# Kernel tuning notes

Measured on AMD Instinct MI355X. Metric: run time of the kernel, lower is better.

Reference implementation:

```python
import jax, jax.numpy as jnp
import numpy as np

NEG_SLOPE = 0.01  # torch F.leaky_relu default

def _lrelu(x):
    return jax.nn.leaky_relu(x, NEG_SLOPE)

def setup_inputs() -> dict:
    key = jax.random.key(0)
    ks = jax.random.split(key, 24)
    B, N, E = 512, 20000, 640000
    n_enc_1, n_enc_2, n_z = 512, 256, 64
    n_dec_2, n_dec_1, hidden = 256, 512, 256
    p = lambda k, shp, fan: jax.random.normal(k, shp, jnp.float32) * (1.0 / np.sqrt(fan))
    return {
        "data": jax.random.normal(ks[0], (B, N), jnp.float32),
        "noise": jax.random.normal(ks[1], (B, N), jnp.float32),
        "edge_index": jax.random.randint(ks[2], (2, E), 0, N, jnp.int32),
        "w_gcn": jax.random.normal(ks[3], (), jnp.float32),
        "b_gcn": jax.random.normal(ks[4], (), jnp.float32) * 0.1,
        "enc1_w": p(ks[5], (N, n_enc_1), N), "enc1_b": p(ks[6], (n_enc_1,), N),
        "enc2_w": p(ks[7], (n_enc_1, n_enc_2), n_enc_1), "enc2_b": p(ks[8], (n_enc_2,), n_enc_1),
        "enc3_w": p(ks[9], (n_enc_2, n_z), n_enc_2), "enc3_b": p(ks[10], (n_z,), n_enc_2),
        "dec1_w": p(ks[11], (n_z, n_dec_2), n_z), "dec1_b": p(ks[12], (n_dec_2,), n_z),
        "dec2_w": p(ks[13], (n_dec_2, n_dec_1), n_dec_2), "dec2_b": p(ks[14], (n_dec_1,), n_dec_2),
        "dec3_w": p(ks[15], (n_dec_1, N), n_dec_1), "dec3_b": p(ks[16], (N,), n_dec_1),
        "disc1_w": p(ks[17], (n_z, hidden), n_z), "disc1_b": p(ks[18], (hidden,), n_z),
        "disc2_w": p(ks[19], (hidden, hidden), hidden), "disc2_b": p(ks[20], (hidden,), hidden),
        "disc3_w": p(ks[21], (hidden, 1), hidden), "disc3_b": p(ks[22], (1,), hidden),
    }

def _gcn_batched(x, edge_index, w_gcn, b_gcn):
    # x: [B, N] -> GCNConv(1,1, improved=True) applied per row, vectorized.
    B, N = x.shape
    src, dst = edge_index[0], edge_index[1]
    loop = jnp.arange(N, dtype=src.dtype)
    src_a = jnp.concatenate([src, loop])
    dst_a = jnp.concatenate([dst, loop])
    # improved=True: self-loop edge weight 2.0
    ew = jnp.concatenate([jnp.ones(src.shape[0], x.dtype), jnp.full((N,), 2.0, x.dtype)])
    deg = jax.ops.segment_sum(ew, dst_a, num_segments=N)
    dinv = jnp.where(deg > 0, jax.lax.rsqrt(deg), 0.0)
    norm = dinv[src_a] * ew * dinv[dst_a]  # [E+N]
    xl = x * w_gcn                         # lin (1x1 weight, no bias)
    msgs = xl[:, src_a] * norm[None, :]    # [B, E+N]
    agg = jnp.zeros_like(x).at[:, dst_a].add(msgs)
    return agg + b_gcn

def reference(data, noise, edge_index, w_gcn, b_gcn,
              enc1_w, enc1_b, enc2_w, enc2_b, enc3_w, enc3_b,
              dec1_w, dec1_b, dec2_w, dec2_b, dec3_w, dec3_b,
              disc1_w, disc1_b, disc2_w, disc2_b, disc3_w, disc3_b):
    x = data + noise * 0.1
    gcn_out = _lrelu(_gcn_batched(x, edge_index, w_gcn, b_gcn))  # [B, N]
    h1 = _lrelu(gcn_out @ enc1_w + enc1_b)
    h2 = _lrelu(h1 @ enc2_w + enc2_b)
    z = _lrelu(h2 @ enc3_w + enc3_b)
    d1 = _lrelu(z @ dec1_w + dec1_b)
    d2 = _lrelu(d1 @ dec2_w + dec2_b)
    dec_h3 = _lrelu(d2 @ dec3_w + dec3_b)
    g1 = _lrelu(z @ disc1_w + disc1_b)
    g2 = _lrelu(g1 @ disc2_w + disc2_b)
    d = jax.nn.sigmoid(g2 @ disc3_w + disc3_b)
    return (dec_h3, z, d)
```

## Files before the change

### kernel.cpp

```cpp
#include <hip/hip_runtime.h>
#include <hip/hip_bf16.h>


#define LRELU(v) ((v) > 0.f ? (v) : 0.01f * (v))

static constexpr int Bb = 512;
static constexpr int Nn = 20000;
static constexpr int Ee = 640000;
static constexpr int KPAD = 20480;
static constexpr int NPD = 20096;
static constexpr int RSU = 36;
static constexpr int RSW = 18;

typedef __attribute__((ext_vector_type(8))) short short8;
typedef __attribute__((ext_vector_type(4))) short short4v;
typedef __attribute__((ext_vector_type(4))) float f32x4;

__device__ __forceinline__ ushort f2bf(float f) {
  uint u = __builtin_bit_cast(uint, f);
  u = u + 0x7FFFu + ((u >> 16) & 1u);
  return (ushort)(u >> 16);
}
__device__ __forceinline__ float bfLo(uint u) {
  return __builtin_bit_cast(float, u << 16);
}
__device__ __forceinline__ float bfHi(uint u) {
  return __builtin_bit_cast(float, u & 0xffff0000u);
}

__global__ void transpose_xs_k(const float* __restrict__ a, const float* __restrict__ nz,
                               const float* __restrict__ dinv, ushort* __restrict__ xs) {
  __shared__ ushort tile[64][65];
  int c0 = blockIdx.x * 64;
  int p = blockIdx.y;
  int rbase = p * 64;
  for (int i = threadIdx.x; i < 64 * 64; i += 256) {
    int rr = i >> 6, cc = i & 63;
    int r = rbase + rr, c = c0 + cc;
    ushort v = 0;
    if (c < Nn) {
      size_t idx = (size_t)r * Nn + c;
      v = f2bf(dinv[c] * (a[idx] + 0.1f * nz[idx]));
    }
    tile[rr][cc] = v;
  }
  __syncthreads();
  for (int i = threadIdx.x; i < 64 * 64; i += 256) {
    int cc = i >> 6, rr = i & 63;
    int c = c0 + cc;
    if (c < Nn) xs[((size_t)p * Nn + c) * 64 + rr] = tile[rr][cc];
  }
}

__global__ void hist_check_k(const int* __restrict__ src, const int* __restrict__ dst, int E,
                             int* __restrict__ cnt, int* __restrict__ flag) {
  int i = blockIdx.x * 256 + threadIdx.x;
  if (i < E) {
    int s = src[i], d = dst[i];
    if ((unsigned)s >= (unsigned)Nn || (unsigned)d >= (unsigned)Nn) {
      atomicExch(flag, 1);
    } else {
      atomicAdd(&cnt[d], 1);
    }
  }
}

__global__ void offs_k(const int* __restrict__ cnt, int* __restrict__ offs,
                       int* __restrict__ cursor, float* __restrict__ dinv,
                       int* __restrict__ bump) {
  int i = blockIdx.x * 256 + threadIdx.x;
  int l = threadIdx.x & 63;
  int v = (i < Nn) ? cnt[i] : 0;
  int x = v;
#pragma unroll
  for (int d = 1; d < 64; d <<= 1) {
    int t = __shfl_up(x, d);
    if (l >= d) x += t;
  }
  int total = __shfl(x, 63);
  int base = 0;
  if (l == 0) base = atomicAdd(bump, total);
  base = __shfl(base, 0);
  int excl = base + x - v;
  if (i < Nn) {
    offs[i] = excl;
    cursor[i] = excl;
    dinv[i] = rsqrtf(2.0f + (float)v);
  }
}

__global__ void scatter_k(const int* __restrict__ src, const int* __restrict__ dst, int E,
                          int* __restrict__ cursor, uint* __restrict__ eOff) {
  int i = blockIdx.x * 256 + threadIdx.x;
  if (i < E) {
    int s = src[i], d = dst[i];
    if ((unsigned)s >= (unsigned)Nn || (unsigned)d >= (unsigned)Nn) return;
    int p = atomicAdd(&cursor[d], 1);
    eOff[p] = (uint)s * 128u;
  }
}

__global__ __launch_bounds__(256) void spmm_p8_k(
    const ushort* __restrict__ xs, const uint* __restrict__ eOff, const int* __restrict__ offs,
    const int* __restrict__ cnt, const float* __restrict__ dinv, const float* __restrict__ wg,
    const float* __restrict__ bg, ushort* __restrict__ gcnT) {
  __shared__ uint sIdx[4][2][32];
  int bid = blockIdx.x;
  int panel = bid & 7;
  int wv = threadIdx.x >> 6, l = threadIdx.x & 63;
  int h = l >> 5, q = l & 31;
  int n = (bid >> 3) * 8 + wv * 2 + h;
  int o = offs[n], c = cnt[n];
  const char* base = (const char*)(xs + (size_t)panel * Nn * 64) + q * 4;
  const uint* ep = eOff + o;
  uint su = *(const uint*)(base + (size_t)n * 128);
  float a0 = 2.0f * bfLo(su), a1 = 2.0f * bfHi(su);
  float b0 = 0.f, b1 = 0.f;

  for (int bi = 0; bi < c; bi += 32) {
    int rem = c - bi;
    if (rem > 32) rem = 32;
    sIdx[wv][h][q] = (q < rem) ? ep[bi + q] : 0u;
    int i = 0;
    for (; i + 8 <= rem; i += 8) {
      uint u[8];
#pragma unroll
      for (int j = 0; j < 8; ++j) u[j] = *(const uint*)(base + sIdx[wv][h][i + j]);
#pragma unroll
      for (int j = 0; j < 8; j += 2) {
        a0 += bfLo(u[j]);
        a1 += bfHi(u[j]);
        b0 += bfLo(u[j + 1]);
        b1 += bfHi(u[j + 1]);
      }
    }
    for (; i < rem; ++i) {
      uint u = *(const uint*)(base + sIdx[wv][h][i]);
      a0 += bfLo(u);
      a1 += bfHi(u);
    }
  }

  float wdn = wg[0] * dinv[n], bb = bg[0];
  float v0 = wdn * (a0 + b0) + bb;
  float v1 = wdn * (a1 + b1) + bb;
  v0 = LRELU(v0);
  v1 = LRELU(v1);
  uint pk = (uint)f2bf(v0) | ((uint)f2bf(v1) << 16);
  *(uint*)&gcnT[((size_t)panel * KPAD + n) * 64 + 2 * q] = pk;
}

__global__ __launch_bounds__(256) void mfma_gemm3(const ushort* __restrict__ AT,
                                                  const float* __restrict__ B, int ldb, int KB,
                                                  int iters, float* __restrict__ C, int ldc) {
  __shared__ ushort As[128 * RSU];
  __shared__ ushort Bs[128 * RSU];
  int n0 = blockIdx.x * 128, m0 = blockIdx.y * 128;
  int k0 = blockIdx.z * iters * 32;
  int tid = threadIdx.x;
  int kp = tid >> 4;
  int c8 = (tid & 15) * 8;
  int l = tid & 63, w = tid >> 6;
  int wr = w >> 1, wc = w & 1;
  int lrow = l & 15, lkg = l >> 4;
  int gm = m0 + c8;
  const ushort* Ap = AT + (size_t)(gm >> 6) * ((size_t)KPAD * 64) + (gm & 63);
  int bcol = n0 + c8;
  f32x4 acc[4][4] = {};

  uint4 pa0, pa1;
  float4 pb00, pb01, pb10, pb11;

#define GLOAD(KG)                                                              \
  {                                                                            \
    int kq = (KG) + 2 * kp;                                                    \
    pa0 = *(const uint4*)&Ap[(size_t)kq * 64];                                 \
    pa1 = *(const uint4*)&Ap[(size_t)(kq + 1) * 64];                           \
    pb00 = pb01 = pb10 = pb11 = float4{0.f, 0.f, 0.f, 0.f};                    \
    if (kq < KB) {                                                             \
      const float4* bp = (const float4*)(B + (size_t)kq * ldb + bcol);         \
      pb00 = bp[0];                                                            \
      pb01 = bp[1];                                                            \
    }                                                                          \
    if (kq + 1 < KB) {                                                         \
      const float4* bp = (const float4*)(B + (size_t)(kq + 1) * ldb + bcol);   \
      pb10 = bp[0];                                                            \
      pb11 = bp[1];                                                            \
    }                                                                          \
  }

  GLOAD(k0);

  for (int kt = 0; kt < iters; ++kt) {
    uint wa[8], wb[8];
    wa[0] = (pa0.x & 0xffffu) | (pa1.x << 16);
    wa[1] = (pa0.x >> 16) | (pa1.x & 0xffff0000u);
    wa[2] = (pa0.y & 0xffffu) | (pa1.y << 16);
    wa[3] = (pa0.y >> 16) | (pa1.y & 0xffff0000u);
    wa[4] = (pa0.z & 0xffffu) | (pa1.z << 16);
    wa[5] = (pa0.z >> 16) | (pa1.z & 0xffff0000u);
    wa[6] = (pa0.w & 0xffffu) | (pa1.w << 16);
    wa[7] = (pa0.w >> 16) | (pa1.w & 0xffff0000u);
    wb[0] = (uint)f2bf(pb00.x) | ((uint)f2bf(pb10.x) << 16);
    wb[1] = (uint)f2bf(pb00.y) | ((uint)f2bf(pb10.y) << 16);
    wb[2] = (uint)f2bf(pb00.z) | ((uint)f2bf(pb10.z) << 16);
    wb[3] = (uint)f2bf(pb00.w) | ((uint)f2bf(pb10.w) << 16);
    wb[4] = (uint)f2bf(pb01.x) | ((uint)f2bf(pb11.x) << 16);
    wb[5] = (uint)f2bf(pb01.y) | ((uint)f2bf(pb11.y) << 16);
    wb[6] = (uint)f2bf(pb01.z) | ((uint)f2bf(pb11.z) << 16);
    wb[7] = (uint)f2bf(pb01.w) | ((uint)f2bf(pb11.w) << 16);
    __syncthreads();
    {
      uint* aw = (uint*)As;
      uint* bw = (uint*)Bs;
#pragma unroll
      for (int j = 0; j < 8; ++j) {
        aw[(c8 + j) * RSW + kp] = wa[j];
        bw[(c8 + j) * RSW + kp] = wb[j];
      }
    }
    __syncthreads();
    if (kt + 1 < iters) GLOAD(k0 + (kt + 1) * 32);
    short8 a[4], b[4];
#pragma unroll
    for (int mi = 0; mi < 4; ++mi) {
      int m = wr * 64 + mi * 16 + lrow;
      const short4v* p = (const short4v*)&As[m * RSU + lkg * 8];
      a[mi] = __builtin_shufflevector(p[0], p[1], 0, 1, 2, 3, 4, 5, 6, 7);
    }
#pragma unroll
    for (int nj = 0; nj < 4; ++nj) {
      int n = wc * 64 + nj * 16 + lrow;
      const short4v* p = (const short4v*)&Bs[n * RSU + lkg * 8];
      b[nj] = __builtin_shufflevector(p[0], p[1], 0, 1, 2, 3, 4, 5, 6, 7);
    }
#pragma unroll
    for (int mi = 0; mi < 4; ++mi)
#pragma unroll
      for (int nj = 0; nj < 4; ++nj)
        acc[mi][nj] = __builtin_amdgcn_mfma_f32_16x16x32_bf16(a[mi], b[nj], acc[mi][nj], 0, 0, 0);
  }
#undef GLOAD

#pragma unroll
  for (int mi = 0; mi < 4; ++mi)
#pragma unroll
    for (int nj = 0; nj < 4; ++nj)
#pragma unroll
      for (int r = 0; r < 4; ++r) {
        int row = m0 + wr * 64 + mi * 16 + lkg * 4 + r;
        int col = n0 + wc * 64 + nj * 16 + lrow;
        atomicAdd(&C[(size_t)row * ldc + col], acc[mi][nj][r]);
      }
}

__global__ void conv_wf_k(const float* __restrict__ W, ushort* __restrict__ wf) {
  int n = blockIdx.x * 256 + threadIdx.x;
  int kb = blockIdx.y;
  if (n >= NPD) return;
  ushort v[8];
#pragma unroll
  for (int j = 0; j < 8; ++j)
    v[j] = (n < Nn) ? f2bf(W[(size_t)(8 * kb + j) * Nn + n]) : (ushort)0;
  uint4 pk;
  pk.x = (uint)v[0] | ((uint)v[1] << 16);
  pk.y = (uint)v[2] | ((uint)v[3] << 16);
  pk.z = (uint)v[4] | ((uint)v[5] << 16);
  pk.w = (uint)v[6] | ((uint)v[7] << 16);
  *(uint4*)&wf[((size_t)kb * NPD + n) * 8] = pk;
}

__global__ __launch_bounds__(256) void fmg_dec3_k(const ushort* __restrict__ d2f,
                                                  const ushort* __restrict__ wf,
                                                  const float* __restrict__ bias,
                                                  float* __restrict__ C) {
  int n0 = blockIdx.x * 128, m0 = blockIdx.y * 128;
  int l = threadIdx.x & 63, w = threadIdx.x >> 6;
  int wr = w >> 1, wc = w & 1;
  int lrow = l & 15, lkg = l >> 4;
  f32x4 acc[4][4] = {};

#pragma unroll 4
  for (int ks = 0; ks < 16; ++ks) {
    int kb = ks * 4 + lkg;
    short8 a[4], b[4];
#pragma unroll
    for (int mi = 0; mi < 4; ++mi) {
      int m = m0 + wr * 64 + mi * 16 + lrow;
      a[mi] = *(const short8*)&d2f[((size_t)kb * 512 + m) * 8];
    }
#pragma unroll
    for (int nj = 0; nj < 4; ++nj) {
      int n = n0 + wc * 64 + nj * 16 + lrow;
      b[nj] = *(const short8*)&wf[((size_t)kb * NPD + n) * 8];
    }
#pragma unroll
    for (int mi = 0; mi < 4; ++mi)
#pragma unroll
      for (int nj = 0; nj < 4; ++nj)
        acc[mi][nj] = __builtin_amdgcn_mfma_f32_16x16x32_bf16(a[mi], b[nj], acc[mi][nj], 0, 0, 0);
  }

#pragma unroll
  for (int mi = 0; mi < 4; ++mi)
#pragma unroll
    for (int nj = 0; nj < 4; ++nj)
#pragma unroll
      for (int r = 0; r < 4; ++r) {
        int row = m0 + wr * 64 + mi * 16 + lkg * 4 + r;
        int col = n0 + wc * 64 + nj * 16 + lrow;
        if (col < Nn) {
          float v = acc[mi][nj][r] + bias[col];
          C[(size_t)row * Nn + col] = LRELU(v);
        }
      }
}

__global__ __launch_bounds__(256) void tail2_k(
    const float* __restrict__ h1, const float* __restrict__ c1, const float* __restrict__ W2,
    const float* __restrict__ c2, const float* __restrict__ W3, const float* __restrict__ c3,
    const float* __restrict__ Wd1, const float* __restrict__ cd1, const float* __restrict__ Wd2,
    const float* __restrict__ cd2, const float* __restrict__ Wg1, const float* __restrict__ cg1,
    const float* __restrict__ Wg2, const float* __restrict__ cg2, const float* __restrict__ Wg3,
    const float* __restrict__ cg3, float* __restrict__ out_z, float* __restrict__ out_d,
    ushort* __restrict__ d2f) {
  __shared__ float s_h1[512];
  __shared__ float s_h2[256];
  __shared__ float s_z[64];
  __shared__ float s_d1[256];
  __shared__ float s_g1[256];
  __shared__ float s_g2[256];
  __shared__ float s_part[4][256];
  __shared__ float s_red[4];
  int rl = blockIdx.x;
  int t = threadIdx.x;
  int w = t >> 6, l = t & 63;

  {
    float r0 = h1[(size_t)rl * 512 + t] + c1[t];
    float r1 = h1[(size_t)rl * 512 + t + 256] + c1[t + 256];
    s_h1[t] = LRELU(r0);
    s_h1[t + 256] = LRELU(r1);
  }
  __syncthreads();

  {
    int c4 = l * 4;
    float a0 = 0.f, a1 = 0.f, a2 = 0.f, a3 = 0.f;
#pragma unroll 8
    for (int k = w * 128; k < w * 128 + 128; ++k) {
      float4 wv = *(const float4*)&W2[(size_t)k * 256 + c4];
      float x = s_h1[k];
      a0 += x * wv.x; a1 += x * wv.y; a2 += x * wv.z; a3 += x * wv.w;
    }
    float4 pv = {a0, a1, a2, a3};
    *(float4*)&s_part[w][c4] = pv;
  }
  __syncthreads();
  s_h2[t] = LRELU(s_part[0][t] + s_part[1][t] + s_part[2][t] + s_part[3][t] + c2[t]);
  __syncthreads();

  {
    int c = t >> 2, p = t & 3;
    float a = 0.f;
#pragma unroll 8
    for (int k = p * 64; k < p * 64 + 64; ++k) a += s_h2[k] * W3[(size_t)k * 64 + c];
    s_part[p][c] = a;
  }
  __syncthreads();
  if (t < 64) {
    float v = s_part[0][t] + s_part[1][t] + s_part[2][t] + s_part[3][t] + c3[t];
    v = LRELU(v);
    s_z[t] = v;
    out_z[(size_t)rl * 64 + t] = v;
  }
  __syncthreads();

  {
    float a = 0.f;
#pragma unroll
    for (int k = 0; k < 64; ++k) a += s_z[k] * Wd1[(size_t)k * 256 + t];
    s_d1[t] = LRELU(a + cd1[t]);
  }
  {
    float a = 0.f;
#pragma unroll
    for (int k = 0; k < 64; ++k) a += s_z[k] * Wg1[(size_t)k * 256 + t];
    s_g1[t] = LRELU(a + cg1[t]);
  }
  __syncthreads();

  {
    int g = t & 127, p = t >> 7;
    int c4 = g * 4;
    float a0 = 0.f, a1 = 0.f, a2 = 0.f, a3 = 0.f;
#pragma unroll 8
    for (int k = p * 128; k < p * 128 + 128; ++k) {
      float4 wv = *(const float4*)&Wd2[(size_t)k * 512 + c4];
      float x = s_d1[k];
      a0 += x * wv.x; a1 += x * wv.y; a2 += x * wv.z; a3 += x * wv.w;
    }
    float* sp = &s_part[0][0];
    float4 pv = {a0, a1, a2, a3};
    *(float4*)&sp[p * 512 + c4] = pv;
  }
  __syncthreads();
  {
    const float* sp = &s_part[0][0];
#pragma unroll
    for (int cc = 0; cc < 2; ++cc) {
      int c = t + cc * 256;
      float v = sp[c] + sp[512 + c] + cd2[c];
      v = LRELU(v);
      d2f[((size_t)(c >> 3) * 512 + rl) * 8 + (c & 7)] = f2bf(v);
    }
  }
  __syncthreads();

  {
    int c4 = l * 4;
    float a0 = 0.f, a1 = 0.f, a2 = 0.f, a3 = 0.f;
#pragma unroll 8
    for (int k = w * 64; k < w * 64 + 64; ++k) {
      float4 wv = *(const float4*)&Wg2[(size_t)k * 256 + c4];
      float x = s_g1[k];
      a0 += x * wv.x; a1 += x * wv.y; a2 += x * wv.z; a3 += x * wv.w;
    }
    float4 pv = {a0, a1, a2, a3};
    *(float4*)&s_part[w][c4] = pv;
  }
  __syncthreads();
  s_g2[t] = LRELU(s_part[0][t] + s_part[1][t] + s_part[2][t] + s_part[3][t] + cg2[t]);
  __syncthreads();

  {
    float p = s_g2[t] * Wg3[t];
#pragma unroll
    for (int o = 32; o > 0; o >>= 1) p += __shfl_down(p, o);
    if ((t & 63) == 0) s_red[t >> 6] = p;
    __syncthreads();
    if (t == 0) {
      float s = s_red[0] + s_red[1] + s_red[2] + s_red[3] + cg3[0];
      out_d[rl] = 1.f / (1.f + __expf(-s));
    }
  }
}

__global__ void sentinel_k(float* out, float val) { out[0] = val; }
__global__ void flag_sentinel_k(float* out, const int* flag) {
  if (*flag != 0) out[0] = 70000.0f;
}

extern "C" void kernel_launch(void* const* d_in, const int* in_sizes, int n_in,
                              void* d_out, int out_size, void* d_ws, size_t ws_size,
                              hipStream_t stream) {
  const float* data = (const float*)d_in[0];
  const float* noise = (const float*)d_in[1];
  const int* edge = (const int*)d_in[2];
  const int* esrc_in = edge;
  const int* edst_in = edge + Ee;
  const float* w_gcn = (const float*)d_in[3];
  const float* b_gcn = (const float*)d_in[4];
  const float* enc1_w = (const float*)d_in[5];
  const float* enc1_b = (const float*)d_in[6];
  const float* enc2_w = (const float*)d_in[7];
  const float* enc2_b = (const float*)d_in[8];
  const float* enc3_w = (const float*)d_in[9];
  const float* enc3_b = (const float*)d_in[10];
  const float* dec1_w = (const float*)d_in[11];
  const float* dec1_b = (const float*)d_in[12];
  const float* dec2_w = (const float*)d_in[13];
  const float* dec2_b = (const float*)d_in[14];
  const float* dec3_w = (const float*)d_in[15];
  const float* dec3_b = (const float*)d_in[16];
  const float* disc1_w = (const float*)d_in[17];
  const float* disc1_b = (const float*)d_in[18];
  const float* disc2_w = (const float*)d_in[19];
  const float* disc2_b = (const float*)d_in[20];
  const float* disc3_w = (const float*)d_in[21];
  const float* disc3_b = (const float*)d_in[22];

  char* w = (char*)d_ws;
  size_t o = 0;
  auto alloc = [&](size_t bytes) {
    size_t r = o;
    o = (o + bytes + 15) & ~(size_t)15;
    return r;
  };
  size_t r1 = alloc((size_t)64 * NPD * 8 * 2);
  ushort* xs = (ushort*)(w + r1);
  ushort* wf = (ushort*)(w + r1);
  ushort* gcnT = (ushort*)(w + alloc((size_t)8 * KPAD * 64 * 2));
  float* h1 = (float*)(w + alloc(512 * 512 * 4));
  ushort* d2f = (ushort*)(w + alloc((size_t)64 * 512 * 8 * 2));
  float* dinv = (float*)(w + alloc(Nn * 4));
  int* cnt = (int*)(w + alloc(Nn * 4));
  int* offs = (int*)(w + alloc(Nn * 4));
  int* cursor = (int*)(w + alloc(Nn * 4));
  uint* eOff = (uint*)(w + alloc(Ee * 4));
  int* flag = (int*)(w + alloc(16));

  float* outp = (float*)d_out;
  float* out_dec = outp;
  float* out_z = outp + (size_t)Bb * Nn;
  float* out_d = out_z + (size_t)Bb * 64;

  static const int expect_sizes[23] = {
      10240000, 10240000, 1280000, 1, 1,
      10240000, 512, 131072, 256, 16384, 64,
      16384, 256, 131072, 512, 10240000, 20000,
      16384, 256, 65536, 256, 256, 1};
  float host_sentinel = 0.f;
  if (n_in != 23) host_sentinel = 50000.f;
  else if (out_size != 10273280) host_sentinel = 80000.f;
  else if (ws_size < 46200000u) host_sentinel = 60000.f;
  else {
    for (int i = 0; i < 23; ++i)
      if (in_sizes[i] != expect_sizes[i]) { host_sentinel = 100000.f + 1000.f * i; break; }
  }

  hipMemsetAsync(cnt, 0, Nn * sizeof(int), stream);
  hipMemsetAsync(flag, 0, 2 * sizeof(int), stream);
  hist_check_k<<<(Ee + 255) / 256, 256, 0, stream>>>(esrc_in, edst_in, Ee, cnt, flag);
  offs_k<<<(Nn + 255) / 256, 256, 0, stream>>>(cnt, offs, cursor, dinv, flag + 1);
  scatter_k<<<(Ee + 255) / 256, 256, 0, stream>>>(esrc_in, edst_in, Ee, cursor, eOff);
  hipMemsetAsync(gcnT, 0, (size_t)8 * KPAD * 64 * 2, stream);

  {
    dim3 g((Nn + 63) / 64, 8);
    transpose_xs_k<<<g, 256, 0, stream>>>(data, noise, dinv, xs);
  }
  spmm_p8_k<<<(Nn / 8) * 8, 256, 0, stream>>>(xs, eOff, offs, cnt, dinv, w_gcn, b_gcn, gcnT);
  hipMemsetAsync(h1, 0, 512 * 512 * 4, stream);
  {
    dim3 g(512 / 128, 512 / 128, 64);
    mfma_gemm3<<<g, 256, 0, stream>>>(gcnT, enc1_w, 512, Nn, 10, h1, 512);
  }
  tail2_k<<<Bb, 256, 0, stream>>>(h1, enc1_b, enc2_w, enc2_b, enc3_w, enc3_b, dec1_w, dec1_b,
                                  dec2_w, dec2_b, disc1_w, disc1_b, disc2_w, disc2_b, disc3_w,
                                  disc3_b, out_z, out_d, d2f);
  {
    dim3 g((NPD + 255) / 256, 64);
    conv_wf_k<<<g, 256, 0, stream>>>(dec3_w, wf);
  }
  {
    dim3 g(NPD / 128, 512 / 128);
    fmg_dec3_k<<<g, 256, 0, stream>>>(d2f, wf, dec3_b, out_dec);
  }

  flag_sentinel_k<<<1, 1, 0, stream>>>(out_dec, flag);
  if (host_sentinel != 0.f) sentinel_k<<<1, 1, 0, stream>>>(out_dec, host_sentinel);
}
```

Baseline: 308.9 us.

## Widen SpMM panels to 128-row chunks and swizzle GEMM LDS writes

Changes the transposed activation layout from 8 panels of 64 batch rows to 4 chunks of 128 rows. Each wavefront now gathers a full 256-byte row per edge, with one node per wave instead of two half-wave nodes. The enc1 GEMM reads the new layout, XOR-swizzles its LDS stores and loads to reduce bank conflicts, and uses split-K 32 with 20 iterations instead of 64 with 10, which halves the atomic adds. The gcnT memset now zeroes only the padding rows. This aims at better gather coalescing, fewer edge-index reads per row, and less LDS contention, at the cost of more work per wave.

```diff
diff --git a/kernel.cpp b/kernel.cpp
--- a/kernel.cpp
+++ b/kernel.cpp
@@ -33,6 +33,8 @@
   __shared__ ushort tile[64][65];
   int c0 = blockIdx.x * 64;
   int p = blockIdx.y;
+  int chunk = p >> 1;
+  int sub = (p & 1) * 64;
   int rbase = p * 64;
   for (int i = threadIdx.x; i < 64 * 64; i += 256) {
     int rr = i >> 6, cc = i & 63;
@@ -48,7 +50,7 @@
   for (int i = threadIdx.x; i < 64 * 64; i += 256) {
     int cc = i >> 6, rr = i & 63;
     int c = c0 + cc;
-    if (c < Nn) xs[((size_t)p * Nn + c) * 64 + rr] = tile[rr][cc];
+    if (c < Nn) xs[(size_t)chunk * Nn * 128 + (size_t)c * 128 + sub + rr] = tile[rr][cc];
   }
 }
 
@@ -96,76 +98,77 @@
     int s = src[i], d = dst[i];
     if ((unsigned)s >= (unsigned)Nn || (unsigned)d >= (unsigned)Nn) return;
     int p = atomicAdd(&cursor[d], 1);
-    eOff[p] = (uint)s * 128u;
-  }
-}
-
-__global__ __launch_bounds__(256) void spmm_p8_k(
+    eOff[p] = (uint)s * 256u;
+  }
+}
+
+__global__ __launch_bounds__(256) void spmm_chunk_k(
     const ushort* __restrict__ xs, const uint* __restrict__ eOff, const int* __restrict__ offs,
     const int* __restrict__ cnt, const float* __restrict__ dinv, const float* __restrict__ wg,
     const float* __restrict__ bg, ushort* __restrict__ gcnT) {
-  __shared__ uint sIdx[4][2][32];
+  __shared__ uint sIdx[4][64];
   int bid = blockIdx.x;
-  int panel = bid & 7;
+  int chunk = bid & 3;
+  int ngrp = bid >> 2;
   int wv = threadIdx.x >> 6, l = threadIdx.x & 63;
-  int h = l >> 5, q = l & 31;
-  int n = (bid >> 3) * 8 + wv * 2 + h;
+  int n = ngrp * 4 + wv;
   int o = offs[n], c = cnt[n];
-  const char* base = (const char*)(xs + (size_t)panel * Nn * 64) + q * 4;
+  const char* base = (const char*)(xs + (size_t)chunk * Nn * 128) + l * 4;
   const uint* ep = eOff + o;
-  uint su = *(const uint*)(base + (size_t)n * 128);
-  float a0 = 2.0f * bfLo(su), a1 = 2.0f * bfHi(su);
-  float b0 = 0.f, b1 = 0.f;
-
-  for (int bi = 0; bi < c; bi += 32) {
+  uint su = *(const uint*)(base + (size_t)n * 256);
+  float a00 = 2.0f * bfLo(su), a01 = 2.0f * bfHi(su);
+  float a10 = 0.f, a11 = 0.f;
+
+  for (int bi = 0; bi < c; bi += 64) {
     int rem = c - bi;
-    if (rem > 32) rem = 32;
-    sIdx[wv][h][q] = (q < rem) ? ep[bi + q] : 0u;
+    if (rem > 64) rem = 64;
+    sIdx[wv][l] = (l < rem) ? ep[bi + l] : 0u;
     int i = 0;
     for (; i + 8 <= rem; i += 8) {
       uint u[8];
 #pragma unroll
-      for (int j = 0; j < 8; ++j) u[j] = *(const uint*)(base + sIdx[wv][h][i + j]);
+      for (int j = 0; j < 8; ++j) u[j] = *(const uint*)(base + sIdx[wv][i + j]);
 #pragma unroll
       for (int j = 0; j < 8; j += 2) {
-        a0 += bfLo(u[j]);
-        a1 += bfHi(u[j]);
-        b0 += bfLo(u[j + 1]);
-        b1 += bfHi(u[j + 1]);
+        a00 += bfLo(u[j]);
+        a01 += bfHi(u[j]);
+        a10 += bfLo(u[j + 1]);
+        a11 += bfHi(u[j + 1]);
       }
     }
     for (; i < rem; ++i) {
-      uint u = *(const uint*)(base + sIdx[wv][h][i]);
-      a0 += bfLo(u);
-      a1 += bfHi(u);
+      uint u = *(const uint*)(base + sIdx[wv][i]);
+      a00 += bfLo(u);
+      a01 += bfHi(u);
     }
   }
 
   float wdn = wg[0] * dinv[n], bb = bg[0];
-  float v0 = wdn * (a0 + b0) + bb;
-  float v1 = wdn * (a1 + b1) + bb;
+  float v0 = wdn * (a00 + a10) + bb;
+  float v1 = wdn * (a01 + a11) + bb;
   v0 = LRELU(v0);
   v1 = LRELU(v1);
   uint pk = (uint)f2bf(v0) | ((uint)f2bf(v1) << 16);
-  *(uint*)&gcnT[((size_t)panel * KPAD + n) * 64 + 2 * q] = pk;
-}
-
-__global__ __launch_bounds__(256) void mfma_gemm3(const ushort* __restrict__ AT,
-                                                  const float* __restrict__ B, int ldb, int KB,
-                                                  int iters, float* __restrict__ C, int ldc) {
+  *(uint*)&gcnT[(size_t)chunk * KPAD * 128 + (size_t)n * 128 + 2 * l] = pk;
+}
+
+__global__ __launch_bounds__(256) void mfma_gemm4(const ushort* __restrict__ AT,
+                                                  const float* __restrict__ B, int KB,
+                                                  int iters, float* __restrict__ C) {
   __shared__ ushort As[128 * RSU];
   __shared__ ushort Bs[128 * RSU];
   int n0 = blockIdx.x * 128, m0 = blockIdx.y * 128;
   int k0 = blockIdx.z * iters * 32;
   int tid = threadIdx.x;
   int kp = tid >> 4;
-  int c8 = (tid & 15) * 8;
+  int cpr = tid & 15;
+  int c8 = cpr * 8;
   int l = tid & 63, w = tid >> 6;
   int wr = w >> 1, wc = w & 1;
   int lrow = l & 15, lkg = l >> 4;
-  int gm = m0 + c8;
-  const ushort* Ap = AT + (size_t)(gm >> 6) * ((size_t)KPAD * 64) + (gm & 63);
+  const ushort* Ap = AT + (size_t)(m0 >> 7) * ((size_t)KPAD * 128);
   int bcol = n0 + c8;
+  int kps = kp ^ (((cpr >> 1) & 3) << 2);
   f32x4 acc[4][4] = {};
 
   uint4 pa0, pa1;
@@ -174,16 +177,16 @@
 #define GLOAD(KG)                                                              \
   {                                                                            \
     int kq = (KG) + 2 * kp;                                                    \
-    pa0 = *(const uint4*)&Ap[(size_t)kq * 64];                                 \
-    pa1 = *(const uint4*)&Ap[(size_t)(kq + 1) * 64];                           \
+    pa0 = *(const uint4*)&Ap[(size_t)kq * 128 + c8];                           \
+    pa1 = *(const uint4*)&Ap[(size_t)(kq + 1) * 128 + c8];                     \
     pb00 = pb01 = pb10 = pb11 = float4{0.f, 0.f, 0.f, 0.f};                    \
     if (kq < KB) {                                                             \
-      const float4* bp = (const float4*)(B + (size_t)kq * ldb + bcol);         \
+      const float4* bp = (const float4*)(B + (size_t)kq * 512 + bcol);         \
       pb00 = bp[0];                                                            \
       pb01 = bp[1];                                                            \
     }                                                                          \
     if (kq + 1 < KB) {                                                         \
-      const float4* bp = (const float4*)(B + (size_t)(kq + 1) * ldb + bcol);   \
+      const float4* bp = (const float4*)(B + (size_t)(kq + 1) * 512 + bcol);   \
       pb10 = bp[0];                                                            \
       pb11 = bp[1];                                                            \
     }                                                                          \
@@ -215,8 +218,8 @@
       uint* bw = (uint*)Bs;
 #pragma unroll
       for (int j = 0; j < 8; ++j) {
-        aw[(c8 + j) * RSW + kp] = wa[j];
-        bw[(c8 + j) * RSW + kp] = wb[j];
+        aw[(c8 + j) * RSW + kps] = wa[j];
+        bw[(c8 + j) * RSW + kps] = wb[j];
       }
     }
     __syncthreads();
@@ -225,13 +228,15 @@
 #pragma unroll
     for (int mi = 0; mi < 4; ++mi) {
       int m = wr * 64 + mi * 16 + lrow;
-      const short4v* p = (const short4v*)&As[m * RSU + lkg * 8];
+      int lk2 = lkg ^ ((wr * 4 + mi) & 3);
+      const short4v* p = (const short4v*)&As[m * RSU + lk2 * 8];
       a[mi] = __builtin_shufflevector(p[0], p[1], 0, 1, 2, 3, 4, 5, 6, 7);
     }
 #pragma unroll
     for (int nj = 0; nj < 4; ++nj) {
       int n = wc * 64 + nj * 16 + lrow;
-      const short4v* p = (const short4v*)&Bs[n * RSU + lkg * 8];
+      int lk2 = lkg ^ ((wc * 4 + nj) & 3);
+      const short4v* p = (const short4v*)&Bs[n * RSU + lk2 * 8];
       b[nj] = __builtin_shufflevector(p[0], p[1], 0, 1, 2, 3, 4, 5, 6, 7);
     }
 #pragma unroll
@@ -250,7 +255,7 @@
       for (int r = 0; r < 4; ++r) {
         int row = m0 + wr * 64 + mi * 16 + lkg * 4 + r;
         int col = n0 + wc * 64 + nj * 16 + lrow;
-        atomicAdd(&C[(size_t)row * ldc + col], acc[mi][nj][r]);
+        atomicAdd(&C[(size_t)row * 512 + col], acc[mi][nj][r]);
       }
 }
 
@@ -490,7 +495,7 @@
   size_t r1 = alloc((size_t)64 * NPD * 8 * 2);
   ushort* xs = (ushort*)(w + r1);
   ushort* wf = (ushort*)(w + r1);
-  ushort* gcnT = (ushort*)(w + alloc((size_t)8 * KPAD * 64 * 2));
+  ushort* gcnT = (ushort*)(w + alloc((size_t)4 * KPAD * 128 * 2));
   float* h1 = (float*)(w + alloc(512 * 512 * 4));
   ushort* d2f = (ushort*)(w + alloc((size_t)64 * 512 * 8 * 2));
   float* dinv = (float*)(w + alloc(Nn * 4));
@@ -513,7 +518,7 @@
   float host_sentinel = 0.f;
   if (n_in != 23) host_sentinel = 50000.f;
   else if (out_size != 10273280) host_sentinel = 80000.f;
-  else if (ws_size < 46200000u) host_sentinel = 60000.f;
+  else if (ws_size < 46100000u) host_sentinel = 60000.f;
   else {
     for (int i = 0; i < 23; ++i)
       if (in_sizes[i] != expect_sizes[i]) { host_sentinel = 100000.f + 1000.f * i; break; }
@@ -524,17 +529,19 @@
   hist_check_k<<<(Ee + 255) / 256, 256, 0, stream>>>(esrc_in, edst_in, Ee, cnt, flag);
   offs_k<<<(Nn + 255) / 256, 256, 0, stream>>>(cnt, offs, cursor, dinv, flag + 1);
   scatter_k<<<(Ee + 255) / 256, 256, 0, stream>>>(esrc_in, edst_in, Ee, cursor, eOff);
-  hipMemsetAsync(gcnT, 0, (size_t)8 * KPAD * 64 * 2, stream);
+  for (int c = 0; c < 4; ++c)
+    hipMemsetAsync(gcnT + ((size_t)c * KPAD + Nn) * 128, 0, (size_t)(KPAD - Nn) * 128 * 2,
+                   stream);
 
   {
     dim3 g((Nn + 63) / 64, 8);
     transpose_xs_k<<<g, 256, 0, stream>>>(data, noise, dinv, xs);
   }
-  spmm_p8_k<<<(Nn / 8) * 8, 256, 0, stream>>>(xs, eOff, offs, cnt, dinv, w_gcn, b_gcn, gcnT);
+  spmm_chunk_k<<<(Nn / 4) * 4, 256, 0, stream>>>(xs, eOff, offs, cnt, dinv, w_gcn, b_gcn, gcnT);
   hipMemsetAsync(h1, 0, 512 * 512 * 4, stream);
   {
-    dim3 g(512 / 128, 512 / 128, 64);
-    mfma_gemm3<<<g, 256, 0, stream>>>(gcnT, enc1_w, 512, Nn, 10, h1, 512);
+    dim3 g(512 / 128, 512 / 128, 32);
+    mfma_gemm4<<<g, 256, 0, stream>>>(gcnT, enc1_w, Nn, 20, h1);
   }
   tail2_k<<<Bb, 256, 0, stream>>>(h1, enc1_b, enc2_w, enc2_b, enc3_w, enc3_b, dec1_w, dec1_b,
                                   dec2_w, dec2_b, disc1_w, disc1_b, disc2_w, disc2_b, disc3_w,
```

New measurement: 288.2 us. 1.07x faster.
